# Performance work log

Hardware: AMD Instinct MI355X
Metric: run time of the kernel (lower is better)

The kernel has to match this reference:

```python
import jax, jax.numpy as jnp
import numpy as np

B, N, E = 4, 8192, 65536
OBS, H, OUT, NOUT = 128, 256, 1024, 18


def setup_inputs() -> dict:
    key = jax.random.key(0)
    ks = jax.random.split(key, 8)
    nodes = jax.random.normal(ks[0], (B, N, OBS), dtype=jnp.float32)
    edges = jax.random.randint(ks[1], (B, 2, E), 0, N, dtype=jnp.int64)
    # Glorot-ish init for weights
    W0 = jax.random.normal(ks[2], (OBS, H), dtype=jnp.float32) / np.float32(np.sqrt(OBS))
    W1 = jax.random.normal(ks[3], (H, OUT), dtype=jnp.float32) / np.float32(np.sqrt(H))
    W_logit = jax.random.normal(ks[4], (OUT, NOUT), dtype=jnp.float32) / np.float32(np.sqrt(OUT))
    W_val = jax.random.normal(ks[5], (OUT, 1), dtype=jnp.float32) / np.float32(np.sqrt(OUT))
    return {
        "nodes": nodes, "edges": edges,
        "W0": W0, "b0": jnp.zeros((H,), jnp.float32),
        "W1": W1, "b1": jnp.zeros((OUT,), jnp.float32),
        "W_logit": W_logit, "b_logit": jnp.zeros((NOUT,), jnp.float32),
        "W_val": W_val, "b_val": jnp.zeros((1,), jnp.float32),
    }


def _gcn_layer(x, src, dst, W, b, n):
    # PyG GCNConv: out = D^{-1/2} (A + I) D^{-1/2} X W + b   (self-loops already in src/dst)
    h = x @ W                                                     # [N, F_out]
    deg = jax.ops.segment_sum(jnp.ones(src.shape, jnp.float32), dst, num_segments=n)
    dinv = jnp.where(deg > 0, jax.lax.rsqrt(deg), 0.0)            # deg^{-1/2}
    norm = dinv[src] * dinv[dst]                                  # [Etot]
    msg = h[src] * norm[:, None]                                  # gather + normalize
    agg = jax.ops.segment_sum(msg, dst, num_segments=n)           # scatter-add
    return agg + b


def reference(nodes, edges, W0, b0, W1, b1, W_logit, b_logit, W_val, b_val):
    n = nodes.shape[1]
    loops = jnp.arange(n, dtype=edges.dtype)  # self-loops, added by GCNConv

    def per_graph(x, ei):
        src = jnp.concatenate([ei[0], loops])
        dst = jnp.concatenate([ei[1], loops])
        h = jax.nn.relu(_gcn_layer(x, src, dst, W0, b0, n))
        # (original applies F.dropout here; omitted for a deterministic reference)
        h = jax.nn.relu(_gcn_layer(h, src, dst, W1, b1, n))
        return h

    out = jax.vmap(per_graph)(nodes, edges)        # [B, N, OUT]
    logits = out @ W_logit + b_logit               # [B, N, NOUT]
    values = (out @ W_val + b_val)[..., 0]         # [B, N]
    return logits, values
```

## Files before the change

kernel.cpp:

```cpp
#include <hip/hip_runtime.h>
#include <hip/hip_bf16.h>

#define BB   4
#define NN   8192
#define EE   65536
#define FOBS 128
#define FH   256
#define FOUT 1024
#define NLOG 18
#define OFFS_STRIDE (NN + 1)
#define P20  20

typedef __attribute__((ext_vector_type(8))) short frag8;
typedef __attribute__((ext_vector_type(4))) float f32x4;

__device__ __forceinline__ ushort f2b(float v) {
    __hip_bfloat16 h = __float2bfloat16(v);
    return *reinterpret_cast<ushort*>(&h);
}
__device__ __forceinline__ float b2f(ushort u) { return __uint_as_float(((uint)u) << 16); }
__device__ __forceinline__ float blo(uint u) { return __uint_as_float(u << 16); }
__device__ __forceinline__ float bhi(uint u) { return __uint_as_float(u & 0xffff0000u); }

__global__ void count_kernel(const int* __restrict__ edges, int* __restrict__ cnt) {
    int g = blockIdx.y;
    int i = blockIdx.x * blockDim.x + threadIdx.x;
    const int* dst = edges + (size_t)g * 2 * EE + EE;
    if (i < EE) atomicAdd(&cnt[(size_t)g * NN + dst[i]], 1);
}

__global__ __launch_bounds__(1024) void scan_kernel(const int* __restrict__ cnt_all,
                                                    int* __restrict__ offs_all,
                                                    int* __restrict__ cursor_all,
                                                    float* __restrict__ dinv_all) {
    int g = blockIdx.x;
    const int* cnt = cnt_all + (size_t)g * NN;
    int* offs = offs_all + (size_t)g * OFFS_STRIDE;
    int* cursor = cursor_all + (size_t)g * NN;
    float* dinv = dinv_all + (size_t)g * NN;

    int t = threadIdx.x;
    int base = t * 8;
    int v[8], s = 0;
#pragma unroll
    for (int j = 0; j < 8; ++j) {
        v[j] = cnt[base + j];
        s += v[j];
        dinv[base + j] = rsqrtf((float)v[j] + 1.0f);
    }
    int lane = t & 63, w = t >> 6;
    int pre = s;
#pragma unroll
    for (int d = 1; d < 64; d <<= 1) {
        int x = __shfl_up(pre, d, 64);
        if (lane >= d) pre += x;
    }
    __shared__ int wsum[16];
    if (lane == 63) wsum[w] = pre;
    __syncthreads();
    if (t == 0) {
        int run = 0;
#pragma unroll
        for (int i = 0; i < 16; ++i) { int tmp = wsum[i]; wsum[i] = run; run += tmp; }
    }
    __syncthreads();
    int excl = wsum[w] + (pre - s);
#pragma unroll
    for (int j = 0; j < 8; ++j) {
        offs[base + j] = excl;
        cursor[base + j] = excl;
        excl += v[j];
    }
    if (t == 1023) offs[NN] = excl;
}

__global__ void csr_fill(const int* __restrict__ edges, int* __restrict__ cursor_all,
                         int* __restrict__ csr_all) {
    int g = blockIdx.y;
    int e = blockIdx.x * blockDim.x + threadIdx.x;
    const int* src = edges + (size_t)g * 2 * EE;
    const int* dst = src + EE;
    if (e < EE) {
        int d = dst[e];
        int slot = atomicAdd(&cursor_all[(size_t)g * NN + d], 1);
        csr_all[(size_t)g * EE + slot] = src[e];
    }
}

__global__ __launch_bounds__(256) void gather_agg_f32(
    const float* __restrict__ x_all, const int* __restrict__ offs_all,
    const int* __restrict__ csr_all, const float* __restrict__ dinv_all,
    uint* __restrict__ agg_all)
{
    int g = blockIdx.y;
    int wv = threadIdx.x >> 6, lane = threadIdx.x & 63;
    int n = blockIdx.x * 4 + wv;
    const float2* x = (const float2*)(x_all + (size_t)g * NN * FOBS);
    const int* offs = offs_all + (size_t)g * OFFS_STRIDE;
    const int* csr = csr_all + (size_t)g * EE;
    const float* dinv = dinv_all + (size_t)g * NN;

    float wn = dinv[n];
    float2 self = x[(size_t)n * 64 + lane];
    float ax = wn * wn * self.x, ay = wn * wn * self.y;

    int i0 = offs[n], i1 = offs[n + 1];
    int i = i0;
    for (; i + 4 <= i1; i += 4) {
        int s0 = csr[i], s1 = csr[i + 1], s2 = csr[i + 2], s3 = csr[i + 3];
        float w0 = dinv[s0] * wn, w1 = dinv[s1] * wn, w2 = dinv[s2] * wn, w3 = dinv[s3] * wn;
        float2 r0 = x[(size_t)s0 * 64 + lane];
        float2 r1 = x[(size_t)s1 * 64 + lane];
        float2 r2 = x[(size_t)s2 * 64 + lane];
        float2 r3 = x[(size_t)s3 * 64 + lane];
        ax += w0 * r0.x + w1 * r1.x + w2 * r2.x + w3 * r3.x;
        ay += w0 * r0.y + w1 * r1.y + w2 * r2.y + w3 * r3.y;
    }
    for (; i < i1; ++i) {
        int s = csr[i];
        float w = dinv[s] * wn;
        float2 r = x[(size_t)s * 64 + lane];
        ax += w * r.x; ay += w * r.y;
    }
    agg_all[((size_t)g * NN + n) * 64 + lane] = (uint)f2b(ax) | ((uint)f2b(ay) << 16);
}

__global__ __launch_bounds__(256) void gather_agg_bf16(
    const uint2* __restrict__ xb_all, const int* __restrict__ offs_all,
    const int* __restrict__ csr_all, const float* __restrict__ dinv_all,
    uint2* __restrict__ agg_all)
{
    int g = blockIdx.y;
    int wv = threadIdx.x >> 6, lane = threadIdx.x & 63;
    int n = blockIdx.x * 4 + wv;
    const uint2* xb = xb_all + (size_t)g * NN * 64;
    const int* offs = offs_all + (size_t)g * OFFS_STRIDE;
    const int* csr = csr_all + (size_t)g * EE;
    const float* dinv = dinv_all + (size_t)g * NN;

    float wn = dinv[n];
    uint2 u = xb[(size_t)n * 64 + lane];
    float w2 = wn * wn;
    float a0 = w2 * blo(u.x), a1 = w2 * bhi(u.x), a2 = w2 * blo(u.y), a3 = w2 * bhi(u.y);

    int i0 = offs[n], i1 = offs[n + 1];
    int i = i0;
    for (; i + 4 <= i1; i += 4) {
        int s0 = csr[i], s1 = csr[i + 1], s2 = csr[i + 2], s3 = csr[i + 3];
        float w0 = dinv[s0] * wn, w1 = dinv[s1] * wn, ww2 = dinv[s2] * wn, w3 = dinv[s3] * wn;
        uint2 r0 = xb[(size_t)s0 * 64 + lane];
        uint2 r1 = xb[(size_t)s1 * 64 + lane];
        uint2 r2 = xb[(size_t)s2 * 64 + lane];
        uint2 r3 = xb[(size_t)s3 * 64 + lane];
        a0 += w0 * blo(r0.x) + w1 * blo(r1.x) + ww2 * blo(r2.x) + w3 * blo(r3.x);
        a1 += w0 * bhi(r0.x) + w1 * bhi(r1.x) + ww2 * bhi(r2.x) + w3 * bhi(r3.x);
        a2 += w0 * blo(r0.y) + w1 * blo(r1.y) + ww2 * blo(r2.y) + w3 * blo(r3.y);
        a3 += w0 * bhi(r0.y) + w1 * bhi(r1.y) + ww2 * bhi(r2.y) + w3 * bhi(r3.y);
    }
    for (; i < i1; ++i) {
        int s = csr[i];
        float w = dinv[s] * wn;
        uint2 r = xb[(size_t)s * 64 + lane];
        a0 += w * blo(r.x); a1 += w * bhi(r.x);
        a2 += w * blo(r.y); a3 += w * bhi(r.y);
    }
    uint2 o;
    o.x = (uint)f2b(a0) | ((uint)f2b(a1) << 16);
    o.y = (uint)f2b(a2) | ((uint)f2b(a3) << 16);
    agg_all[((size_t)g * NN + n) * 64 + lane] = o;
}

__global__ void w_transpose_cast(const float* __restrict__ W, ushort* __restrict__ WT,
                                 int K, int N) {
    int i = blockIdx.x * blockDim.x + threadIdx.x;
    if (i < K * N) {
        int n = i / K, k = i - n * K;
        WT[i] = f2b(W[(size_t)k * N + n]);
    }
}

__global__ void pack_heads_w(const float* __restrict__ Wl, const float* __restrict__ Wv,
                             ushort* __restrict__ WT19) {
    int i = blockIdx.x * blockDim.x + threadIdx.x;
    if (i < 19 * FOUT) {
        int o = i >> 10, k = i & (FOUT - 1);
        WT19[i] = f2b((o < NLOG) ? Wl[(size_t)k * NLOG + o] : Wv[k]);
    }
}

__global__ __launch_bounds__(256) void mfma_gemm(
    const ushort* __restrict__ A_all, const ushort* __restrict__ BT,
    const float* __restrict__ bias, ushort* __restrict__ C_all,
    int M, int N, int K, int relu)
{
    __shared__ ushort As[128][72];
    __shared__ ushort Bs[128][72];

    int g = blockIdx.z;
    const ushort* A = A_all + (size_t)g * M * K;
    ushort* C = C_all + (size_t)g * M * N;

    int t = threadIdx.x;
    int bn = blockIdx.x, bm = blockIdx.y;
    int lane = t & 63, w = t >> 6;
    int wm = w >> 1, wn = w & 1;
    int l15 = lane & 15, quad = lane >> 4;

    f32x4 acc[4][4] = {};

    int srow = t >> 3, scol = (t & 7) * 8;
    const ushort* Abase = A + (size_t)(bm * 128) * K;
    const ushort* Bbase = BT + (size_t)(bn * 128) * K;

    for (int k0 = 0; k0 < K; k0 += 64) {
#pragma unroll
        for (int i = 0; i < 4; ++i) {
            int row = srow + 32 * i;
            *(uint4*)&As[row][scol] = *(const uint4*)(Abase + (size_t)row * K + k0 + scol);
        }
#pragma unroll
        for (int i = 0; i < 4; ++i) {
            int row = srow + 32 * i;
            *(uint4*)&Bs[row][scol] = *(const uint4*)(Bbase + (size_t)row * K + k0 + scol);
        }
        __syncthreads();
#pragma unroll
        for (int kk = 0; kk < 64; kk += 32) {
            frag8 af[4], bf[4];
#pragma unroll
            for (int i = 0; i < 4; ++i)
                af[i] = *(const frag8*)&As[wm * 64 + i * 16 + l15][kk + quad * 8];
#pragma unroll
            for (int j = 0; j < 4; ++j)
                bf[j] = *(const frag8*)&Bs[wn * 64 + j * 16 + l15][kk + quad * 8];
#pragma unroll
            for (int i = 0; i < 4; ++i)
#pragma unroll
                for (int j = 0; j < 4; ++j)
                    acc[i][j] = __builtin_amdgcn_mfma_f32_16x16x32_bf16(af[i], bf[j], acc[i][j], 0, 0, 0);
        }
        __syncthreads();
    }

#pragma unroll
    for (int i = 0; i < 4; ++i) {
#pragma unroll
        for (int j = 0; j < 4; ++j) {
            int col = bn * 128 + wn * 64 + j * 16 + l15;
            float bcol = bias[col];
#pragma unroll
            for (int r = 0; r < 4; ++r) {
                int row = bm * 128 + wm * 64 + i * 16 + quad * 4 + r;
                float v = acc[i][j][r] + bcol;
                if (relu) v = fmaxf(v, 0.0f);
                C[(size_t)row * N + col] = f2b(v);
            }
        }
    }
}

__global__ __launch_bounds__(256) void gemm2_heads(
    const ushort* __restrict__ hagg_all,
    const ushort* __restrict__ W1T,
    const float*  __restrict__ b1,
    const ushort* __restrict__ WT19,
    float* __restrict__ partial)
{
    __shared__ __align__(16) ushort smem[2 * 128 * 72];
    __shared__ __align__(16) ushort wt[20][136];

    ushort* As = smem;
    ushort* Bs = smem + 128 * 72;
    ushort* Ct = smem;

    int bm = blockIdx.x, sp = blockIdx.y, g = blockIdx.z;
    int t = threadIdx.x;
    int lane = t & 63, w = t >> 6;
    int wm = w >> 1, wn = w & 1;
    int l15 = lane & 15, quad = lane >> 4;
    int srow = t >> 3, scol = (t & 7) * 8;

    const ushort* A0 = hagg_all + ((size_t)g * NN + bm * 128) * FH;

    if (t < 136) wt[19][t] = 0;

    f32x4 hacc[2][2] = {};

    for (int bi = 0; bi < 4; ++bi) {
        int bn = sp * 4 + bi;
        __syncthreads();

        for (int idx = t; idx < 19 * 16; idx += 256) {
            int row = idx >> 4, c8 = (idx & 15) * 8;
            *(uint4*)&wt[row][c8] = *(const uint4*)(WT19 + (size_t)row * FOUT + bn * 128 + c8);
        }

        f32x4 acc[4][4] = {};
        const ushort* Bbase = W1T + (size_t)(bn * 128) * FH;

        for (int k0 = 0; k0 < FH; k0 += 64) {
#pragma unroll
            for (int i = 0; i < 4; ++i) {
                int row = srow + 32 * i;
                *(uint4*)&As[row * 72 + scol] = *(const uint4*)(A0 + (size_t)row * FH + k0 + scol);
                *(uint4*)&Bs[row * 72 + scol] = *(const uint4*)(Bbase + (size_t)row * FH + k0 + scol);
            }
            __syncthreads();
#pragma unroll
            for (int kk = 0; kk < 64; kk += 32) {
                frag8 af[4], bf[4];
#pragma unroll
                for (int i = 0; i < 4; ++i)
                    af[i] = *(const frag8*)&As[(wm * 64 + i * 16 + l15) * 72 + kk + quad * 8];
#pragma unroll
                for (int j = 0; j < 4; ++j)
                    bf[j] = *(const frag8*)&Bs[(wn * 64 + j * 16 + l15) * 72 + kk + quad * 8];
#pragma unroll
                for (int i = 0; i < 4; ++i)
#pragma unroll
                    for (int j = 0; j < 4; ++j)
                        acc[i][j] = __builtin_amdgcn_mfma_f32_16x16x32_bf16(af[i], bf[j], acc[i][j], 0, 0, 0);
            }
            __syncthreads();
        }

#pragma unroll
        for (int j = 0; j < 4; ++j) {
            int colL = wn * 64 + j * 16 + l15;
            float bcol = b1[bn * 128 + colL];
#pragma unroll
            for (int i = 0; i < 4; ++i) {
                int rowL = wm * 64 + i * 16 + quad * 4;
#pragma unroll
                for (int r = 0; r < 4; ++r) {
                    float v = fmaxf(acc[i][j][r] + bcol, 0.0f);
                    Ct[(size_t)(rowL + r) * 136 + colL] = f2b(v);
                }
            }
        }
        __syncthreads();

        int r1 = (l15 < 3) ? (16 + l15) : 19;
#pragma unroll
        for (int kk = 0; kk < 128; kk += 32) {
            frag8 b0 = *(const frag8*)&wt[l15][kk + quad * 8];
            frag8 bO = *(const frag8*)&wt[r1][kk + quad * 8];
#pragma unroll
            for (int mt = 0; mt < 2; ++mt) {
                int row = (w * 2 + mt) * 16 + l15;
                frag8 af = *(const frag8*)&Ct[(size_t)row * 136 + kk + quad * 8];
                hacc[mt][0] = __builtin_amdgcn_mfma_f32_16x16x32_bf16(af, b0, hacc[mt][0], 0, 0, 0);
                hacc[mt][1] = __builtin_amdgcn_mfma_f32_16x16x32_bf16(af, bO, hacc[mt][1], 0, 0, 0);
            }
        }
    }

#pragma unroll
    for (int mt = 0; mt < 2; ++mt) {
#pragma unroll
        for (int r = 0; r < 4; ++r) {
            int node = bm * 128 + (w * 2 + mt) * 16 + quad * 4 + r;
            size_t base = ((size_t)(sp * BB + g) * NN + node) * P20;
            partial[base + l15] = hacc[mt][0][r];
            if (l15 < 3) partial[base + 16 + l15] = hacc[mt][1][r];
        }
    }
}

__global__ void heads_combine(const float* __restrict__ partial,
                              const float* __restrict__ bl, const float* __restrict__ bv,
                              float* __restrict__ out_logits, float* __restrict__ out_values) {
    int i = blockIdx.x * blockDim.x + threadIdx.x;
    if (i >= BB * NN * 19) return;
    int o = i % 19;
    int gn = i / 19;
    float v = partial[(size_t)gn * P20 + o] + partial[((size_t)BB * NN + gn) * P20 + o];
    if (o < NLOG) out_logits[(size_t)gn * NLOG + o] = v + bl[o];
    else          out_values[gn] = v + bv[0];
}

extern "C" void kernel_launch(void* const* d_in, const int* in_sizes, int n_in,
                              void* d_out, int out_size, void* d_ws, size_t ws_size,
                              hipStream_t stream) {
    const float* nodes = (const float*)d_in[0];
    const int*   edges = (const int*)d_in[1];
    const float* W0 = (const float*)d_in[2];
    const float* b0 = (const float*)d_in[3];
    const float* W1 = (const float*)d_in[4];
    const float* b1 = (const float*)d_in[5];
    const float* Wl = (const float*)d_in[6];
    const float* bl = (const float*)d_in[7];
    const float* Wv = (const float*)d_in[8];
    const float* bv = (const float*)d_in[9];

    float* out_logits = (float*)d_out;
    float* out_values = out_logits + (size_t)BB * NN * NLOG;

    char* ws = (char*)d_ws;
    int*    cnt     = (int*)(ws);
    int*    offs    = (int*)(ws + (128 << 10));
    int*    cursor  = (int*)(ws + (260 << 10));
    float*  dinv    = (float*)(ws + (388 << 10));
    int*    csr_src = (int*)(ws + (516 << 10));
    ushort* W0T     = (ushort*)(ws + (1540 << 10));
    ushort* W1T     = (ushort*)(ws + (1604 << 10));
    ushort* WT19    = (ushort*)(ws + (2116 << 10));
    ushort* xagg_b  = (ushort*)(ws + (4u << 20));
    ushort* h1b     = (ushort*)(ws + (12u << 20));
    ushort* hagg_b  = (ushort*)(ws + (28u << 20));
    float*  partial = (float*)(ws + (44u << 20));

    w_transpose_cast<<<(FOBS * FH + 255) / 256, 256, 0, stream>>>(W0, W0T, FOBS, FH);
    w_transpose_cast<<<(FH * FOUT + 255) / 256, 256, 0, stream>>>(W1, W1T, FH, FOUT);
    pack_heads_w<<<(19 * FOUT + 255) / 256, 256, 0, stream>>>(Wl, Wv, WT19);

    hipMemsetAsync(cnt, 0, (size_t)BB * NN * sizeof(int), stream);
    count_kernel<<<dim3(EE / 256, BB), 256, 0, stream>>>(edges, cnt);
    scan_kernel<<<BB, 1024, 0, stream>>>(cnt, offs, cursor, dinv);
    csr_fill<<<dim3(EE / 256, BB), 256, 0, stream>>>(edges, cursor, csr_src);

    gather_agg_f32<<<dim3(NN / 4, BB), 256, 0, stream>>>(nodes, offs, csr_src, dinv,
                                                         (uint*)xagg_b);
    mfma_gemm<<<dim3(FH / 128, NN / 128, BB), 256, 0, stream>>>(
        xagg_b, W0T, b0, h1b, NN, FH, FOBS, 1);

    gather_agg_bf16<<<dim3(NN / 4, BB), 256, 0, stream>>>((const uint2*)h1b, offs, csr_src,
                                                          dinv, (uint2*)hagg_b);

    gemm2_heads<<<dim3(NN / 128, 2, BB), 256, 0, stream>>>(hagg_b, W1T, b1, WT19, partial);
    heads_combine<<<(BB * NN * 19 + 255) / 256, 256, 0, stream>>>(partial, bl, bv,
                                                                  out_logits, out_values);
}
```

Measured before the change: 205.1 us.

## Pre-cast node features to bf16, merge weight prep kernels, unroll gathers by eight

Adds a single prep kernel that casts the node features to bf16 and transposes and casts all weights, replacing three separate weight kernels. The first-layer gather then reads bf16 rows instead of fp32, halving its random-access traffic. Both gather kernels now use an 8-wide unrolled loop with clamped indices and zeroed weights in place of a 4-wide loop plus scalar tail, which keeps more loads in flight. The cost is an extra full pass over the nodes tensor to cast it, and the input features are rounded to bf16 before aggregation rather than after.

```diff
diff --git a/kernel.cpp b/kernel.cpp
--- a/kernel.cpp
+++ b/kernel.cpp
@@ -18,9 +18,46 @@
     __hip_bfloat16 h = __float2bfloat16(v);
     return *reinterpret_cast<ushort*>(&h);
 }
-__device__ __forceinline__ float b2f(ushort u) { return __uint_as_float(((uint)u) << 16); }
 __device__ __forceinline__ float blo(uint u) { return __uint_as_float(u << 16); }
 __device__ __forceinline__ float bhi(uint u) { return __uint_as_float(u & 0xffff0000u); }
+
+#define CAST_N (BB * NN * FOBS / 4)
+#define W0_N   (FOBS * FH)
+#define W1_N   (FH * FOUT)
+#define WH_N   (19 * FOUT)
+#define PREP_TOTAL (CAST_N + W0_N + W1_N + WH_N)
+
+__global__ void prep_kernel(const float* __restrict__ nodes, ushort* __restrict__ nodes_b,
+                            const float* __restrict__ W0, ushort* __restrict__ W0T,
+                            const float* __restrict__ W1, ushort* __restrict__ W1T,
+                            const float* __restrict__ Wl, const float* __restrict__ Wv,
+                            ushort* __restrict__ WT19) {
+    int idx = blockIdx.x * blockDim.x + threadIdx.x;
+    if (idx < CAST_N) {
+        float4 v = *(const float4*)(nodes + 4 * (size_t)idx);
+        ushort4 o;
+        o.x = f2b(v.x); o.y = f2b(v.y); o.z = f2b(v.z); o.w = f2b(v.w);
+        *(ushort4*)(nodes_b + 4 * (size_t)idx) = o;
+        return;
+    }
+    idx -= CAST_N;
+    if (idx < W0_N) {
+        int n = idx / FOBS, k = idx - n * FOBS;
+        W0T[idx] = f2b(W0[(size_t)k * FH + n]);
+        return;
+    }
+    idx -= W0_N;
+    if (idx < W1_N) {
+        int n = idx / FH, k = idx - n * FH;
+        W1T[idx] = f2b(W1[(size_t)k * FOUT + n]);
+        return;
+    }
+    idx -= W1_N;
+    if (idx < WH_N) {
+        int o = idx >> 10, k = idx & (FOUT - 1);
+        WT19[idx] = f2b((o < NLOG) ? Wl[(size_t)k * NLOG + o] : Wv[k]);
+    }
+}
 
 __global__ void count_kernel(const int* __restrict__ edges, int* __restrict__ cnt) {
     int g = blockIdx.y;
@@ -87,45 +124,51 @@
     }
 }
 
-__global__ __launch_bounds__(256) void gather_agg_f32(
-    const float* __restrict__ x_all, const int* __restrict__ offs_all,
+__global__ __launch_bounds__(256) void gather_agg_b128(
+    const uint* __restrict__ xb_all, const int* __restrict__ offs_all,
     const int* __restrict__ csr_all, const float* __restrict__ dinv_all,
     uint* __restrict__ agg_all)
 {
     int g = blockIdx.y;
     int wv = threadIdx.x >> 6, lane = threadIdx.x & 63;
     int n = blockIdx.x * 4 + wv;
-    const float2* x = (const float2*)(x_all + (size_t)g * NN * FOBS);
+    const uint* xb = xb_all + (size_t)g * NN * 64;
     const int* offs = offs_all + (size_t)g * OFFS_STRIDE;
     const int* csr = csr_all + (size_t)g * EE;
     const float* dinv = dinv_all + (size_t)g * NN;
 
     float wn = dinv[n];
-    float2 self = x[(size_t)n * 64 + lane];
-    float ax = wn * wn * self.x, ay = wn * wn * self.y;
+    uint u = xb[(size_t)n * 64 + lane];
+    float a0 = wn * wn * blo(u), a1 = wn * wn * bhi(u);
 
     int i0 = offs[n], i1 = offs[n + 1];
-    int i = i0;
-    for (; i + 4 <= i1; i += 4) {
-        int s0 = csr[i], s1 = csr[i + 1], s2 = csr[i + 2], s3 = csr[i + 3];
-        float w0 = dinv[s0] * wn, w1 = dinv[s1] * wn, w2 = dinv[s2] * wn, w3 = dinv[s3] * wn;
-        float2 r0 = x[(size_t)s0 * 64 + lane];
-        float2 r1 = x[(size_t)s1 * 64 + lane];
-        float2 r2 = x[(size_t)s2 * 64 + lane];
-        float2 r3 = x[(size_t)s3 * 64 + lane];
-        ax += w0 * r0.x + w1 * r1.x + w2 * r2.x + w3 * r3.x;
-        ay += w0 * r0.y + w1 * r1.y + w2 * r2.y + w3 * r3.y;
-    }
-    for (; i < i1; ++i) {
-        int s = csr[i];
-        float w = dinv[s] * wn;
-        float2 r = x[(size_t)s * 64 + lane];
-        ax += w * r.x; ay += w * r.y;
-    }
-    agg_all[((size_t)g * NN + n) * 64 + lane] = (uint)f2b(ax) | ((uint)f2b(ay) << 16);
-}
-
-__global__ __launch_bounds__(256) void gather_agg_bf16(
+    for (int i = i0; i < i1; i += 8) {
+        int last = i1 - 1;
+        int idx0 = i,     idx1 = min(i + 1, last), idx2 = min(i + 2, last), idx3 = min(i + 3, last);
+        int idx4 = min(i + 4, last), idx5 = min(i + 5, last), idx6 = min(i + 6, last), idx7 = min(i + 7, last);
+        int s0 = csr[idx0], s1 = csr[idx1], s2 = csr[idx2], s3 = csr[idx3];
+        int s4 = csr[idx4], s5 = csr[idx5], s6 = csr[idx6], s7 = csr[idx7];
+        float w0 = dinv[s0] * wn;
+        float w1 = (i + 1 < i1) ? dinv[s1] * wn : 0.0f;
+        float w2 = (i + 2 < i1) ? dinv[s2] * wn : 0.0f;
+        float w3 = (i + 3 < i1) ? dinv[s3] * wn : 0.0f;
+        float w4 = (i + 4 < i1) ? dinv[s4] * wn : 0.0f;
+        float w5 = (i + 5 < i1) ? dinv[s5] * wn : 0.0f;
+        float w6 = (i + 6 < i1) ? dinv[s6] * wn : 0.0f;
+        float w7 = (i + 7 < i1) ? dinv[s7] * wn : 0.0f;
+        uint r0 = xb[(size_t)s0 * 64 + lane], r1 = xb[(size_t)s1 * 64 + lane];
+        uint r2 = xb[(size_t)s2 * 64 + lane], r3 = xb[(size_t)s3 * 64 + lane];
+        uint r4 = xb[(size_t)s4 * 64 + lane], r5 = xb[(size_t)s5 * 64 + lane];
+        uint r6 = xb[(size_t)s6 * 64 + lane], r7 = xb[(size_t)s7 * 64 + lane];
+        a0 += w0 * blo(r0) + w1 * blo(r1) + w2 * blo(r2) + w3 * blo(r3)
+            + w4 * blo(r4) + w5 * blo(r5) + w6 * blo(r6) + w7 * blo(r7);
+        a1 += w0 * bhi(r0) + w1 * bhi(r1) + w2 * bhi(r2) + w3 * bhi(r3)
+            + w4 * bhi(r4) + w5 * bhi(r5) + w6 * bhi(r6) + w7 * bhi(r7);
+    }
+    agg_all[((size_t)g * NN + n) * 64 + lane] = (uint)f2b(a0) | ((uint)f2b(a1) << 16);
+}
+
+__global__ __launch_bounds__(256) void gather_agg_b256(
     const uint2* __restrict__ xb_all, const int* __restrict__ offs_all,
     const int* __restrict__ csr_all, const float* __restrict__ dinv_all,
     uint2* __restrict__ agg_all)
@@ -140,52 +183,41 @@
 
     float wn = dinv[n];
     uint2 u = xb[(size_t)n * 64 + lane];
-    float w2 = wn * wn;
-    float a0 = w2 * blo(u.x), a1 = w2 * bhi(u.x), a2 = w2 * blo(u.y), a3 = w2 * bhi(u.y);
+    float w2s = wn * wn;
+    float a0 = w2s * blo(u.x), a1 = w2s * bhi(u.x), a2 = w2s * blo(u.y), a3 = w2s * bhi(u.y);
 
     int i0 = offs[n], i1 = offs[n + 1];
-    int i = i0;
-    for (; i + 4 <= i1; i += 4) {
-        int s0 = csr[i], s1 = csr[i + 1], s2 = csr[i + 2], s3 = csr[i + 3];
-        float w0 = dinv[s0] * wn, w1 = dinv[s1] * wn, ww2 = dinv[s2] * wn, w3 = dinv[s3] * wn;
-        uint2 r0 = xb[(size_t)s0 * 64 + lane];
-        uint2 r1 = xb[(size_t)s1 * 64 + lane];
-        uint2 r2 = xb[(size_t)s2 * 64 + lane];
-        uint2 r3 = xb[(size_t)s3 * 64 + lane];
-        a0 += w0 * blo(r0.x) + w1 * blo(r1.x) + ww2 * blo(r2.x) + w3 * blo(r3.x);
-        a1 += w0 * bhi(r0.x) + w1 * bhi(r1.x) + ww2 * bhi(r2.x) + w3 * bhi(r3.x);
-        a2 += w0 * blo(r0.y) + w1 * blo(r1.y) + ww2 * blo(r2.y) + w3 * blo(r3.y);
-        a3 += w0 * bhi(r0.y) + w1 * bhi(r1.y) + ww2 * bhi(r2.y) + w3 * bhi(r3.y);
-    }
-    for (; i < i1; ++i) {
-        int s = csr[i];
-        float w = dinv[s] * wn;
-        uint2 r = xb[(size_t)s * 64 + lane];
-        a0 += w * blo(r.x); a1 += w * bhi(r.x);
-        a2 += w * blo(r.y); a3 += w * bhi(r.y);
+    for (int i = i0; i < i1; i += 8) {
+        int last = i1 - 1;
+        int idx0 = i,     idx1 = min(i + 1, last), idx2 = min(i + 2, last), idx3 = min(i + 3, last);
+        int idx4 = min(i + 4, last), idx5 = min(i + 5, last), idx6 = min(i + 6, last), idx7 = min(i + 7, last);
+        int s0 = csr[idx0], s1 = csr[idx1], s2 = csr[idx2], s3 = csr[idx3];
+        int s4 = csr[idx4], s5 = csr[idx5], s6 = csr[idx6], s7 = csr[idx7];
+        float w0 = dinv[s0] * wn;
+        float w1 = (i + 1 < i1) ? dinv[s1] * wn : 0.0f;
+        float w2 = (i + 2 < i1) ? dinv[s2] * wn : 0.0f;
+        float w3 = (i + 3 < i1) ? dinv[s3] * wn : 0.0f;
+        float w4 = (i + 4 < i1) ? dinv[s4] * wn : 0.0f;
+        float w5 = (i + 5 < i1) ? dinv[s5] * wn : 0.0f;
+        float w6 = (i + 6 < i1) ? dinv[s6] * wn : 0.0f;
+        float w7 = (i + 7 < i1) ? dinv[s7] * wn : 0.0f;
+        uint2 r0 = xb[(size_t)s0 * 64 + lane], r1 = xb[(size_t)s1 * 64 + lane];
+        uint2 r2 = xb[(size_t)s2 * 64 + lane], r3 = xb[(size_t)s3 * 64 + lane];
+        uint2 r4 = xb[(size_t)s4 * 64 + lane], r5 = xb[(size_t)s5 * 64 + lane];
+        uint2 r6 = xb[(size_t)s6 * 64 + lane], r7 = xb[(size_t)s7 * 64 + lane];
+        a0 += w0 * blo(r0.x) + w1 * blo(r1.x) + w2 * blo(r2.x) + w3 * blo(r3.x)
+            + w4 * blo(r4.x) + w5 * blo(r5.x) + w6 * blo(r6.x) + w7 * blo(r7.x);
+        a1 += w0 * bhi(r0.x) + w1 * bhi(r1.x) + w2 * bhi(r2.x) + w3 * bhi(r3.x)
+            + w4 * bhi(r4.x) + w5 * bhi(r5.x) + w6 * bhi(r6.x) + w7 * bhi(r7.x);
+        a2 += w0 * blo(r0.y) + w1 * blo(r1.y) + w2 * blo(r2.y) + w3 * blo(r3.y)
+            + w4 * blo(r4.y) + w5 * blo(r5.y) + w6 * blo(r6.y) + w7 * blo(r7.y);
+        a3 += w0 * bhi(r0.y) + w1 * bhi(r1.y) + w2 * bhi(r2.y) + w3 * bhi(r3.y)
+            + w4 * bhi(r4.y) + w5 * bhi(r5.y) + w6 * bhi(r6.y) + w7 * bhi(r7.y);
     }
     uint2 o;
     o.x = (uint)f2b(a0) | ((uint)f2b(a1) << 16);
     o.y = (uint)f2b(a2) | ((uint)f2b(a3) << 16);
     agg_all[((size_t)g * NN + n) * 64 + lane] = o;
-}
-
-__global__ void w_transpose_cast(const float* __restrict__ W, ushort* __restrict__ WT,
-                                 int K, int N) {
-    int i = blockIdx.x * blockDim.x + threadIdx.x;
-    if (i < K * N) {
-        int n = i / K, k = i - n * K;
-        WT[i] = f2b(W[(size_t)k * N + n]);
-    }
-}
-
-__global__ void pack_heads_w(const float* __restrict__ Wl, const float* __restrict__ Wv,
-                             ushort* __restrict__ WT19) {
-    int i = blockIdx.x * blockDim.x + threadIdx.x;
-    if (i < 19 * FOUT) {
-        int o = i >> 10, k = i & (FOUT - 1);
-        WT19[i] = f2b((o < NLOG) ? Wl[(size_t)k * NLOG + o] : Wv[k]);
-    }
 }
 
 __global__ __launch_bounds__(256) void mfma_gemm(
@@ -409,22 +441,22 @@
     ushort* h1b     = (ushort*)(ws + (12u << 20));
     ushort* hagg_b  = (ushort*)(ws + (28u << 20));
     float*  partial = (float*)(ws + (44u << 20));
-
-    w_transpose_cast<<<(FOBS * FH + 255) / 256, 256, 0, stream>>>(W0, W0T, FOBS, FH);
-    w_transpose_cast<<<(FH * FOUT + 255) / 256, 256, 0, stream>>>(W1, W1T, FH, FOUT);
-    pack_heads_w<<<(19 * FOUT + 255) / 256, 256, 0, stream>>>(Wl, Wv, WT19);
+    ushort* nodes_b = (ushort*)(ws + (50u << 20));
+
+    prep_kernel<<<(PREP_TOTAL + 255) / 256, 256, 0, stream>>>(
+        nodes, nodes_b, W0, W0T, W1, W1T, Wl, Wv, WT19);
 
     hipMemsetAsync(cnt, 0, (size_t)BB * NN * sizeof(int), stream);
     count_kernel<<<dim3(EE / 256, BB), 256, 0, stream>>>(edges, cnt);
     scan_kernel<<<BB, 1024, 0, stream>>>(cnt, offs, cursor, dinv);
     csr_fill<<<dim3(EE / 256, BB), 256, 0, stream>>>(edges, cursor, csr_src);
 
-    gather_agg_f32<<<dim3(NN / 4, BB), 256, 0, stream>>>(nodes, offs, csr_src, dinv,
-                                                         (uint*)xagg_b);
+    gather_agg_b128<<<dim3(NN / 4, BB), 256, 0, stream>>>((const uint*)nodes_b, offs, csr_src,
+                                                          dinv, (uint*)xagg_b);
     mfma_gemm<<<dim3(FH / 128, NN / 128, BB), 256, 0, stream>>>(
         xagg_b, W0T, b0, h1b, NN, FH, FOBS, 1);
 
-    gather_agg_bf16<<<dim3(NN / 4, BB), 256, 0, stream>>>((const uint2*)h1b, offs, csr_src,
+    gather_agg_b256<<<dim3(NN / 4, BB), 256, 0, stream>>>((const uint2*)h1b, offs, csr_src,
                                                           dinv, (uint2*)hagg_b);
 
     gemm2_heads<<<dim3(NN / 128, 2, BB), 256, 0, stream>>>(hagg_b, W1T, b1, WT19, partial);
```

After: 209.8 us. 2.3% more time.
